# Optimization experiments

Measured on AMD Instinct MI355X. Metric: run time of the kernel, lower is better.

The kernel has to match this reference:

```python
import jax, jax.numpy as jnp
import numpy as np

B, T, D, U = 64, 512, 512, 1024


def setup_inputs() -> dict:
    key = jax.random.key(0)
    k1, k2, k3 = jax.random.split(key, 3)
    x = jax.random.normal(k1, (B, T, D), dtype=jnp.float32)
    kernel = jax.random.normal(k2, (D, 4 * U), dtype=jnp.float32) * (1.0 / np.sqrt(D))
    rec_kernel = jax.random.normal(k3, (U, 4 * U), dtype=jnp.float32) * (1.0 / np.sqrt(U))
    return {"x": x, "kernel": kernel, "rec_kernel": rec_kernel}


def reference(x, kernel, rec_kernel):
    """SimpleLSTM forward: returns last hidden state h_T of shape [B, U].
    Gate order along the 4U axis is (i, f, c, o), matching the kernel split.
    No biases; initial h and c are zeros (as in the original call()).
    """
    units = rec_kernel.shape[0]
    # Precompute input contributions for all timesteps in one big GEMM:
    # x_gates[b, t, :] == x[b, t] @ kernel  (same math as 4 per-gate matmuls)
    x_gates = jnp.einsum('btd,dk->tbk', x, kernel)  # [T, B, 4U]

    def step(carry, xt):
        h, c = carry
        z = xt + h @ rec_kernel  # [B, 4U]
        i = jax.nn.sigmoid(z[:, :units])
        f = jax.nn.sigmoid(z[:, units:2 * units])
        g = jnp.tanh(z[:, 2 * units:3 * units])
        o = jax.nn.sigmoid(z[:, 3 * units:])
        c_new = f * c + i * g
        h_new = o * jnp.tanh(c_new)
        return (h_new, c_new), None

    batch = x.shape[0]
    h0 = jnp.zeros((batch, units), dtype=x.dtype)
    c0 = jnp.zeros((batch, units), dtype=x.dtype)
    (h_last, _), _ = jax.lax.scan(step, (h0, c0), x_gates)
    return h_last
```

## Files before the change

### kernel.cpp

```cpp
#include <hip/hip_runtime.h>
#include <stdint.h>

#define WS_XB   0LL
#define WS_H    33554432LL
#define WS_FLAG 33816576LL

typedef unsigned short u16;
typedef unsigned int   u32;
typedef unsigned long long u64;
typedef __attribute__((ext_vector_type(8))) short short8;
typedef __attribute__((ext_vector_type(4))) float f32x4;

__device__ __forceinline__ u16 f2bf(float f) {
  unsigned u = __float_as_uint(f);
  u += 0x7FFFu + ((u >> 16) & 1u);
  return (u16)(u >> 16);
}
__device__ __forceinline__ float fast_tanh(float x) {
  float e = __expf(2.f * x);
  return 1.f - 2.f / (e + 1.f);
}

__global__ void conv_x(const float* __restrict__ x, u16* __restrict__ xb) {
  long gid = (long)blockIdx.x * blockDim.x + threadIdx.x;
  long sr = gid >> 6;
  int  d0 = (int)(gid & 63) * 8;
  int  b = (int)(sr >> 9), t = (int)(sr & 511);
  const float* src = x + sr * 512 + d0;
  float4 v0 = *(const float4*)(src);
  float4 v1 = *(const float4*)(src + 4);
  u16 tmp[8] = {f2bf(v0.x), f2bf(v0.y), f2bf(v0.z), f2bf(v0.w),
                f2bf(v1.x), f2bf(v1.y), f2bf(v1.z), f2bf(v1.w)};
  *(short8*)(xb + ((long)t * 64 + b) * 512 + d0) = *(short8*)tmp;
}

__launch_bounds__(256, 1)
__global__ void lstm_fused(const float* __restrict__ kern, const float* __restrict__ rec,
                           const u16* __restrict__ xb, u32* __restrict__ hbuf,
                           u32* __restrict__ flags, float* __restrict__ out) {
  __shared__ u16   smH[2][32 * 64 * 8];
  __shared__ float zscr[4][16][20];

  const int bid = blockIdx.x;
  const int bg = bid >> 6;
  const int ut = bid & 63;
  const int tid = threadIdx.x;
  const int w = tid >> 6, lane = tid & 63;
  const int quad = lane >> 4, n15 = lane & 15;
  const int gate = n15 >> 2, uu = n15 & 3;
  const int rowE = quad * 4 + gate;

  short8 wf[48];
  const size_t gcol = (size_t)gate * 1024 + (size_t)ut * 16 + (size_t)(w * 4 + uu);
#pragma unroll
  for (int ks = 0; ks < 32; ++ks) {
    u16 tmp[8];
#pragma unroll
    for (int j = 0; j < 8; ++j)
      tmp[j] = f2bf(rec[(size_t)(ks * 32 + quad * 8 + j) * 4096 + gcol]);
    wf[ks] = *(short8*)tmp;
  }
#pragma unroll
  for (int ks = 0; ks < 16; ++ks) {
    u16 tmp[8];
#pragma unroll
    for (int j = 0; j < 8; ++j)
      tmp[j] = f2bf(kern[(size_t)(ks * 32 + quad * 8 + j) * 4096 + gcol]);
    wf[32 + ks] = *(short8*)tmp;
  }

  float c = 0.f;

#pragma unroll
  for (int j = 0; j < 8; ++j)
    *(uint4*)(&smH[0][(tid + j * 256) * 8]) = (uint4){0u, 0u, 0u, 0u};

  short8 xf[16];
  {
    const u16* xr = xb + (size_t)(bg * 16 + n15) * 512 + quad * 8;
#pragma unroll
    for (int ks = 0; ks < 16; ++ks) xf[ks] = *(const short8*)(xr + ks * 32);
  }
  f32x4 acc0 = {0.f, 0.f, 0.f, 0.f}, acc1 = {0.f, 0.f, 0.f, 0.f};
#pragma unroll
  for (int ks = 0; ks < 16; ks += 2) {
    acc0 = __builtin_amdgcn_mfma_f32_16x16x32_bf16(xf[ks], wf[32 + ks], acc0, 0, 0, 0);
    acc1 = __builtin_amdgcn_mfma_f32_16x16x32_bf16(xf[ks + 1], wf[33 + ks], acc1, 0, 0, 0);
  }
  __syncthreads();

#define X16_MFMA                                                                   \
  _Pragma("unroll")                                                                \
  for (int ks2 = 0; ks2 < 16; ks2 += 2) {                                          \
    acc0 = __builtin_amdgcn_mfma_f32_16x16x32_bf16(xf[ks2], wf[32 + ks2], acc0, 0, 0, 0);     \
    acc1 = __builtin_amdgcn_mfma_f32_16x16x32_bf16(xf[ks2 + 1], wf[33 + ks2], acc1, 0, 0, 0); \
  }

#define PAYLOAD_LOAD                                                               \
  {                                                                                \
    const u32* hs = hbuf + (size_t)pb * 32768 + (size_t)(bg * 16 + n15) * 512 + quad * 4; \
    _Pragma("unroll")                                                              \
    for (int kk = 0; kk < 8; ++kk) {                                               \
      const u64* src = (const u64*)(hs + (w * 8 + kk) * 16);                       \
      pay[2 * kk]     = __hip_atomic_load(src,     __ATOMIC_RELAXED, __HIP_MEMORY_SCOPE_AGENT); \
      pay[2 * kk + 1] = __hip_atomic_load(src + 1, __ATOMIC_RELAXED, __HIP_MEMORY_SCOPE_AGENT); \
    }                                                                              \
  }

#define OWN8(BASE)                                                                 \
  _Pragma("unroll")                                                                \
  for (int kk = 0; kk < 8; ++kk) {                                                 \
    union { u64 q[2]; short8 s; u32 d[4]; } uo;                                    \
    uo.q[0] = pay[2 * kk]; uo.q[1] = pay[2 * kk + 1];                              \
    if (kk & 1) acc1 = __builtin_amdgcn_mfma_f32_16x16x32_bf16(uo.s, wf[(BASE) + kk], acc1, 0, 0, 0); \
    else        acc0 = __builtin_amdgcn_mfma_f32_16x16x32_bf16(uo.s, wf[(BASE) + kk], acc0, 0, 0, 0); \
    *(uint4*)(smH[pb] + (((BASE) + kk) * 64 + lane) * 8) =                         \
        (uint4){uo.d[0], uo.d[1], uo.d[2], uo.d[3]};                               \
  }

  for (int t = 0; t < 512; ++t) {
    const u16* sh = smH[t & 1];
#pragma unroll
    for (int g = 0; g < 4; ++g) {
      if (g == w) continue;
#pragma unroll
      for (int kk = 0; kk < 8; kk += 2) {
        const int ks = g * 8 + kk;
        short8 a0 = *(const short8*)(sh + (ks * 64 + lane) * 8);
        acc0 = __builtin_amdgcn_mfma_f32_16x16x32_bf16(a0, wf[ks], acc0, 0, 0, 0);
        short8 a1 = *(const short8*)(sh + ((ks + 1) * 64 + lane) * 8);
        acc1 = __builtin_amdgcn_mfma_f32_16x16x32_bf16(a1, wf[ks + 1], acc1, 0, 0, 0);
      }
    }

    const int cw = uu * 4 + gate;
    zscr[w][quad * 4 + 0][cw] = acc0[0] + acc1[0];
    zscr[w][quad * 4 + 1][cw] = acc0[1] + acc1[1];
    zscr[w][quad * 4 + 2][cw] = acc0[2] + acc1[2];
    zscr[w][quad * 4 + 3][cw] = acc0[3] + acc1[3];
    asm volatile("s_waitcnt lgkmcnt(0)" ::: "memory");
    __builtin_amdgcn_sched_barrier(0);
    float4 zv = *(const float4*)&zscr[w][rowE][uu * 4];

    float ig = 1.f / (1.f + __expf(-zv.x));
    float fg = 1.f / (1.f + __expf(-zv.y));
    float gg = fast_tanh(zv.z);
    float og = 1.f / (1.f + __expf(-zv.w));
    c = fg * c + ig * gg;
    float h = og * fast_tanh(c);

    if (t == 511) {
      out[(size_t)(bg * 16 + rowE) * 1024 + (size_t)(ut * 16 + w * 4 + uu)] = h;
      break;
    }

    const int pb = (t + 1) & 1;

    {
      u16 hu = f2bf(h);
      int other = __shfl_xor((int)(unsigned)hu, 1);
      if ((uu & 1) == 0) {
        u32 pw = (u32)hu | ((u32)(unsigned)other << 16);
        __hip_atomic_store(&hbuf[(size_t)pb * 32768 + (size_t)(bg * 16 + rowE) * 512
                                 + ut * 8 + w * 2 + (uu >> 1)],
                           pw, __ATOMIC_RELAXED, __HIP_MEMORY_SCOPE_AGENT);
      }
    }
    __builtin_amdgcn_sched_barrier(0);

    {
      const u16* xr = xb + ((size_t)(t + 1) * 64 + bg * 16 + n15) * 512 + quad * 8;
#pragma unroll
      for (int ks2 = 0; ks2 < 16; ++ks2) xf[ks2] = *(const short8*)(xr + ks2 * 32);
    }
    __builtin_amdgcn_sched_barrier(0);

    asm volatile("s_waitcnt vmcnt(16)" ::: "memory");
    asm volatile("s_barrier" ::: "memory");
    if (tid == 0)
      __hip_atomic_store(&flags[(bg * 64 + ut) * 32], (u32)(t + 1),
                         __ATOMIC_RELAXED, __HIP_MEMORY_SCOPE_AGENT);

    acc0 = (f32x4){0.f, 0.f, 0.f, 0.f};
    acc1 = (f32x4){0.f, 0.f, 0.f, 0.f};

    u64 pay[16];
    if (w == 0) {
      const u32 tgt = (u32)(t + 1);
      const u32* fp = &flags[(bg * 64 + lane) * 32];
      u32 v = __hip_atomic_load(fp, __ATOMIC_RELAXED, __HIP_MEMORY_SCOPE_AGENT);
      while (__ballot(v < tgt) != 0ull) {
        v = __hip_atomic_load(fp, __ATOMIC_RELAXED, __HIP_MEMORY_SCOPE_AGENT);
      }
      PAYLOAD_LOAD;
    } else {
      X16_MFMA;
    }
    asm volatile("s_barrier" ::: "memory");
    if (w == 0) {
      X16_MFMA;
    } else {
      PAYLOAD_LOAD;
    }

    if      (w == 0) { OWN8(0)  }
    else if (w == 1) { OWN8(8)  }
    else if (w == 2) { OWN8(16) }
    else             { OWN8(24) }

    asm volatile("s_waitcnt lgkmcnt(0)" ::: "memory");
    asm volatile("s_barrier" ::: "memory");
  }
}

extern "C" void kernel_launch(void* const* d_in, const int* in_sizes, int n_in,
                              void* d_out, int out_size, void* d_ws, size_t ws_size,
                              hipStream_t stream) {
  const float* x    = (const float*)d_in[0];
  const float* kern = (const float*)d_in[1];
  const float* rec  = (const float*)d_in[2];
  float* out = (float*)d_out;
  char* ws = (char*)d_ws;

  u16* xbp   = (u16*)(ws + WS_XB);
  u32* hbuf  = (u32*)(ws + WS_H);
  u32* flags = (u32*)(ws + WS_FLAG);

  hipMemsetAsync(ws + WS_FLAG, 0, 32768, stream);

  conv_x<<<8192, 256, 0, stream>>>(x, xbp);

  lstm_fused<<<256, 256, 0, stream>>>(kern, rec, xbp, hbuf, flags, out);
}
```

Baseline: 2.940 ms.

## Use per-wave ready flags, drop pre-publish barrier, overlap x-MFMA with payload loads

```diff
diff --git a/kernel.cpp b/kernel.cpp
--- a/kernel.cpp
+++ b/kernel.cpp
@@ -89,9 +89,9 @@
   }
   __syncthreads();
 
-#define X16_MFMA                                                                   \
+#define X8_MFMA(S)                                                                 \
   _Pragma("unroll")                                                                \
-  for (int ks2 = 0; ks2 < 16; ks2 += 2) {                                          \
+  for (int ks2 = (S); ks2 < (S) + 8; ks2 += 2) {                                   \
     acc0 = __builtin_amdgcn_mfma_f32_16x16x32_bf16(xf[ks2], wf[32 + ks2], acc0, 0, 0, 0);     \
     acc1 = __builtin_amdgcn_mfma_f32_16x16x32_bf16(xf[ks2 + 1], wf[33 + ks2], acc1, 0, 0, 0); \
   }
@@ -119,6 +119,7 @@
   }
 
   for (int t = 0; t < 512; ++t) {
+    __builtin_amdgcn_s_setprio(1);
     const u16* sh = smH[t & 1];
 #pragma unroll
     for (int g = 0; g < 4; ++g) {
@@ -155,6 +156,7 @@
     }
 
     const int pb = (t + 1) & 1;
+    const u32 tag = (u32)(t + 1);
 
     {
       u16 hu = f2bf(h);
@@ -176,9 +178,8 @@
     __builtin_amdgcn_sched_barrier(0);
 
     asm volatile("s_waitcnt vmcnt(16)" ::: "memory");
-    asm volatile("s_barrier" ::: "memory");
-    if (tid == 0)
-      __hip_atomic_store(&flags[(bg * 64 + ut) * 32], (u32)(t + 1),
+    if (lane == 0)
+      __hip_atomic_store(&flags[(bg * 64 + ut) * 32 + w], tag,
                          __ATOMIC_RELAXED, __HIP_MEMORY_SCOPE_AGENT);
 
     acc0 = (f32x4){0.f, 0.f, 0.f, 0.f};
@@ -186,27 +187,33 @@
 
     u64 pay[16];
     if (w == 0) {
-      const u32 tgt = (u32)(t + 1);
-      const u32* fp = &flags[(bg * 64 + lane) * 32];
-      u32 v = __hip_atomic_load(fp, __ATOMIC_RELAXED, __HIP_MEMORY_SCOPE_AGENT);
-      while (__ballot(v < tgt) != 0ull) {
-        v = __hip_atomic_load(fp, __ATOMIC_RELAXED, __HIP_MEMORY_SCOPE_AGENT);
+      __builtin_amdgcn_s_setprio(0);
+      const u64* fq = (const u64*)&flags[(bg * 64 + lane) * 32];
+      for (;;) {
+        u64 a = __hip_atomic_load(fq,     __ATOMIC_RELAXED, __HIP_MEMORY_SCOPE_AGENT);
+        u64 b = __hip_atomic_load(fq + 1, __ATOMIC_RELAXED, __HIP_MEMORY_SCOPE_AGENT);
+        u32 mn = min(min((u32)a, (u32)(a >> 32)), min((u32)b, (u32)(b >> 32)));
+        if (__ballot(mn < tag) == 0ull) break;
       }
+      __builtin_amdgcn_s_setprio(1);
       PAYLOAD_LOAD;
     } else {
-      X16_MFMA;
+      X8_MFMA(0);
     }
     asm volatile("s_barrier" ::: "memory");
     if (w == 0) {
-      X16_MFMA;
+      X8_MFMA(0);
+      X8_MFMA(8);
     } else {
       PAYLOAD_LOAD;
+      X8_MFMA(8);
     }
 
     if      (w == 0) { OWN8(0)  }
     else if (w == 1) { OWN8(8)  }
     else if (w == 2) { OWN8(16) }
     else             { OWN8(24) }
+    __builtin_amdgcn_s_setprio(0);
 
     asm volatile("s_waitcnt lgkmcnt(0)" ::: "memory");
     asm volatile("s_barrier" ::: "memory");
```

Result: slower. 3.120 ms (+6.1%).
